# Performance work log

Hardware: AMD Instinct MI355X
Metric: run time of the kernel (lower is better)

The kernel has to match this reference:

```python
import jax, jax.numpy as jnp
import numpy as np

BEAM_WIDTH = 4
BLANK_INDEX = 0
EOS_INDEX = 1


def setup_inputs():
    key = jax.random.key(0)
    k1, k2 = jax.random.split(key)
    T, B, C = 128, 8, 25000
    logits = jax.random.normal(k1, (T, B, C), dtype=jnp.float32)
    seq_len = jnp.full((B,), T, dtype=jnp.int32)
    return {"logits": logits, "seq_len": seq_len}


def _beam_search(logits):
    # logits: [T, B, C]; vectorized form of the per-step beam update:
    #   softmax(beam_score + logits) over C, top-k over (beam, char),
    #   backpointer gather of sequences, per-step re-sort by cumulative log score.
    T, B, C = logits.shape
    W = BEAM_WIDTH
    seqs0 = jnp.full((B, W, T + 1), BLANK_INDEX, dtype=jnp.int32)
    scores0 = jnp.zeros((B, W), dtype=logits.dtype)  # per-step softmax prob score
    logs0 = jnp.zeros((B, W), dtype=logits.dtype)    # accumulated log prob
    active0 = jnp.zeros((B, W), dtype=bool).at[:, 0].set(True)  # start with one beam

    def step(carry, xs):
        scores, logs, seqs, active = carry
        logit_t, t = xs
        # beam score is ADDED to logits before softmax (matches original math)
        expanded = scores[:, :, None] + logit_t[:, None, :]          # [B, W, C]
        probs = jax.nn.softmax(expanded, axis=-1)
        probs = jnp.where(active[:, :, None], probs, -1.0)           # mask inactive beams
        top_p, top_i = jax.lax.top_k(probs.reshape(B, W * C), W)      # [B, W]
        beam_idx = top_i // C                                        # backpointers
        char = (top_i % C).astype(jnp.int32)
        new_logs = jnp.take_along_axis(logs, beam_idx, axis=1) + jnp.log(top_p)
        new_seqs = jnp.take_along_axis(seqs, beam_idx[:, :, None], axis=1)
        # eos is dropped from the sequence in the original; represent as blank
        char_w = jnp.where(char == EOS_INDEX, BLANK_INDEX, char)
        new_seqs = new_seqs.at[:, :, t + 1].set(char_w)
        # per-step re-sort of surviving beams by cumulative log score (desc)
        order = jnp.argsort(-new_logs, axis=1)
        top_p = jnp.take_along_axis(top_p, order, axis=1)
        new_logs = jnp.take_along_axis(new_logs, order, axis=1)
        new_seqs = jnp.take_along_axis(new_seqs, order[:, :, None], axis=1)
        return (top_p, new_logs, new_seqs, jnp.ones_like(active)), None

    (scores, logs, seqs, _), _ = jax.lax.scan(
        step, (scores0, logs0, seqs0, active0), (logits, jnp.arange(T)))
    # final sort by last-step prob score (original sorts by x[0] at the end)
    order = jnp.argsort(-scores, axis=1)
    scores = jnp.take_along_axis(scores, order, axis=1)
    logs = jnp.take_along_axis(logs, order, axis=1)
    seqs = jnp.take_along_axis(seqs, order[:, :, None], axis=1)
    return seqs, scores, logs


def reference(logits, seq_len):
    seqs, scores, logs = _beam_search(logits)
    return seqs, scores, logs
```

## Files before the change

kernel.cpp:

```cpp
#include <hip/hip_runtime.h>
#include <math.h>

#define T_ 128
#define B_ 8
#define C_ 25000
#define W_ 4
#define NROWS (T_ * B_)
#define NT4 (C_ / 4)

__device__ __forceinline__ bool better(float av, int ai, float bv, int bi) {
  return (av > bv) || (av == bv && ai < bi);
}

__global__ __launch_bounds__(512) void rowstats(
    const float* __restrict__ logits,
    float* __restrict__ r_v, int* __restrict__ r_i,
    double* __restrict__ r_p, double* __restrict__ r_lp) {
  const int row = blockIdx.x;
  const float4* __restrict__ x4 =
      reinterpret_cast<const float4*>(logits + (size_t)row * C_);
  const int tid = threadIdx.x;

  float tv[4] = {-INFINITY, -INFINITY, -INFINITY, -INFINITY};
  int ti[4] = {0x7fffffff, 0x7fffffff, 0x7fffffff, 0x7fffffff};
  float s0 = 0.0f, s1 = 0.0f;

  auto ins = [&](float cv, int ci2) {
#pragma unroll
    for (int k = 0; k < 4; ++k) {
      if (better(cv, ci2, tv[k], ti[k])) {
        float t0 = tv[k]; int t1 = ti[k];
        tv[k] = cv; ti[k] = ci2;
        cv = t0; ci2 = t1;
      }
    }
  };

#pragma unroll 4
  for (int i = tid; i < NT4; i += 512) {
    float4 q = x4[i];
    s0 += __expf(q.x) + __expf(q.y);
    s1 += __expf(q.z) + __expf(q.w);
    const int gi = 4 * i;
    if (better(q.x, gi + 0, tv[3], ti[3])) ins(q.x, gi + 0);
    if (better(q.y, gi + 1, tv[3], ti[3])) ins(q.y, gi + 1);
    if (better(q.z, gi + 2, tv[3], ti[3])) ins(q.z, gi + 2);
    if (better(q.w, gi + 3, tv[3], ti[3])) ins(q.w, gi + 3);
  }

  __shared__ float sv[512][4];
  __shared__ int si[512][4];
  __shared__ double ss[512];
#pragma unroll
  for (int k = 0; k < 4; ++k) { sv[tid][k] = tv[k]; si[tid][k] = ti[k]; }
  ss[tid] = (double)s0 + (double)s1;
  __syncthreads();

  for (int off = 256; off > 0; off >>= 1) {
    if (tid < off) {
      ss[tid] += ss[tid + off];
      float a0[4], ov[4]; int a1[4], oi[4];
#pragma unroll
      for (int k = 0; k < 4; ++k) { a0[k] = sv[tid][k]; a1[k] = si[tid][k]; }
      int pa = 0, pb = 0;
#pragma unroll
      for (int k = 0; k < 4; ++k) {
        float bv_ = sv[tid + off][pb]; int bi_ = si[tid + off][pb];
        if (better(a0[pa], a1[pa], bv_, bi_)) { ov[k] = a0[pa]; oi[k] = a1[pa]; ++pa; }
        else { ov[k] = bv_; oi[k] = bi_; ++pb; }
      }
#pragma unroll
      for (int k = 0; k < 4; ++k) { sv[tid][k] = ov[k]; si[tid][k] = oi[k]; }
    }
    __syncthreads();
  }

  if (tid == 0) {
    const int t = row / B_, b = row % B_;
    const int orow = b * T_ + t;
    double den = ss[0];
#pragma unroll
    for (int k = 0; k < 4; ++k) {
      r_v[orow * 4 + k] = sv[0][k];
      r_i[orow * 4 + k] = si[0][k];
      double p = exp((double)sv[0][k]) / den;
      r_p[orow * 4 + k] = p;
      r_lp[orow * 4 + k] = log(p);
    }
  }
}

__global__ __launch_bounds__(64) void beam_sim(
    const float* __restrict__ r_v, const int* __restrict__ r_i,
    const double* __restrict__ r_p, const double* __restrict__ r_lp,
    float* __restrict__ out) {
  const int b = blockIdx.x;
  const int tid = threadIdx.x;

  __shared__ float lv[T_][4];
  __shared__ int lci[T_][4];
  __shared__ double lpk[T_][4];
  __shared__ double lpp[T_][4];
  __shared__ double S[T_];
  __shared__ int Pst[T_][4], Chst[T_][4];
  __shared__ int seq[W_][T_];
  __shared__ double sh_scores[W_], sh_logs[W_];
  __shared__ int sh_ford[W_];

  const size_t base = (size_t)b * T_ * 4;
  for (int e = tid; e < T_ * 4; e += 64) {
    lv[e >> 2][e & 3] = r_v[base + e];
    lci[e >> 2][e & 3] = r_i[base + e];
    lpk[e >> 2][e & 3] = r_lp[base + e];
    lpp[e >> 2][e & 3] = r_p[base + e];
  }
  __syncthreads();

  bool slA = (tid >= 1) &&
      (__float_as_uint(lv[tid][0]) == __float_as_uint(lv[tid][1]));
  bool slB =
      (__float_as_uint(lv[tid + 64][0]) == __float_as_uint(lv[tid + 64][1]));
  const unsigned long long mask0 = __ballot(slA);
  const unsigned long long mask1 = __ballot(slB);

  {
    const int t0 = 2 * tid, t1 = 2 * tid + 1;
    double e0 = (t0 >= 1) ? lpk[t0][0] : 0.0;
    double e1 = lpk[t1][0];
    double pair = e0 + e1;
    double sc = pair;
#pragma unroll
    for (int d = 1; d < 64; d <<= 1) {
      double o = __shfl_up(sc, d, 64);
      if (tid >= d) sc += o;
    }
    double excl = sc - pair;
    S[t0] = excl + e0;
    S[t1] = sc;
  }

  for (int t = tid + 1; t < T_; t += 64) {
    bool slow = (t < 64) ? ((mask0 >> t) & 1ull) : ((mask1 >> (t - 64)) & 1ull);
    if (!slow) {
      int c = lci[t][0];
      seq[0][t] = c; seq[1][t] = c; seq[2][t] = c; seq[3][t] = c;
    }
  }
  __syncthreads();

  if (tid == 0) {
    double logs[4], scor[4] = {0.0, 0.0, 0.0, 0.0};
    for (int j = 0; j < 4; ++j) logs[j] = lpk[0][j];
    int tprev = 0, lastSlow = -1;

    unsigned long long mm = mask0;
    int phase = 0;
    while (true) {
      if (mm == 0) {
        if (phase == 0) { mm = mask1; phase = 1; continue; }
        break;
      }
      int bpos = __builtin_ctzll(mm); mm &= mm - 1;
      int ts = bpos + (phase ? 64 : 0);

      double add = S[ts - 1] - S[tprev];
      for (int j = 0; j < 4; ++j) logs[j] += add;

      float v[4]; int ci[4];
      for (int k = 0; k < 4; ++k) { v[k] = lv[ts][k]; ci[k] = lci[ts][k]; }
      int sw[4], sc_[4], sk[4]; int ns = 0; int k = 0;
      while (ns < 4 && k < 4) {
        int k2 = k;
        while (k2 + 1 < 4 &&
               __float_as_uint(v[k2 + 1]) == __float_as_uint(v[k])) ++k2;
        for (int w = 0; w < 4 && ns < 4; ++w)
          for (int kk = k; kk <= k2 && ns < 4; ++kk) {
            sw[ns] = w; sc_[ns] = ci[kk]; sk[ns] = kk; ++ns;
          }
        k = k2 + 1;
      }
      double nl[4];
      for (int j = 0; j < 4; ++j) nl[j] = logs[sw[j]] + lpk[ts][sk[j]];
      int ord[4] = {0, 1, 2, 3};
      for (int a = 1; a < 4; ++a) {
        int o = ord[a]; int bb = a;
        while (bb > 0 && nl[ord[bb - 1]] < nl[o]) { ord[bb] = ord[bb - 1]; --bb; }
        ord[bb] = o;
      }
      for (int j = 0; j < 4; ++j) {
        Pst[ts][j] = sw[ord[j]];
        Chst[ts][j] = sc_[ord[j]];
      }
      double tl[4];
      for (int j = 0; j < 4; ++j) tl[j] = nl[ord[j]];
      for (int j = 0; j < 4; ++j) logs[j] = tl[j];
      if (ts == T_ - 1)
        for (int j = 0; j < 4; ++j) scor[j] = lpp[ts][sk[ord[j]]];
      tprev = ts;
      lastSlow = ts;
    }
    double add = S[T_ - 1] - S[tprev];
    for (int j = 0; j < 4; ++j) logs[j] += add;
    if (lastSlow != T_ - 1)
      for (int j = 0; j < 4; ++j) scor[j] = lpp[T_ - 1][0];

    float sf[4];
    for (int j = 0; j < 4; ++j) sf[j] = (float)scor[j];
    int ford[4] = {0, 1, 2, 3};
    for (int a = 1; a < 4; ++a) {
      int o = ford[a]; int bb = a;
      while (bb > 0 && sf[ford[bb - 1]] < sf[o]) { ford[bb] = ford[bb - 1]; --bb; }
      ford[bb] = o;
    }
    for (int w = 0; w < 4; ++w) {
      sh_ford[w] = ford[w];
      sh_scores[w] = scor[ford[w]];
      sh_logs[w] = logs[ford[w]];
    }
  }
  __syncthreads();

  if (tid < W_) {
    int j = sh_ford[tid];
    unsigned long long mm = mask1;
    int phase = 1;
    while (true) {
      if (mm == 0) {
        if (phase == 1) { mm = mask0; phase = 0; continue; }
        break;
      }
      int bpos = 63 - __builtin_clzll(mm); mm &= ~(1ull << bpos);
      int ts = bpos + (phase ? 64 : 0);
      seq[tid][ts] = Chst[ts][j];
      j = Pst[ts][j];
    }
    seq[tid][0] = lci[0][j];
  }
  __syncthreads();

  for (int e = tid; e < W_ * (T_ + 1); e += 64) {
    int w = e / (T_ + 1), p = e % (T_ + 1);
    int c = (p == 0) ? 0 : seq[w][p - 1];
    if (c == 1) c = 0;
    out[(size_t)(b * W_ + w) * (T_ + 1) + p] = (float)c;
  }
  if (tid < W_) {
    out[B_ * W_ * (T_ + 1) + b * W_ + tid] = (float)sh_scores[tid];
    out[B_ * W_ * (T_ + 1) + B_ * W_ + b * W_ + tid] = (float)sh_logs[tid];
  }
}

extern "C" void kernel_launch(void* const* d_in, const int* in_sizes, int n_in,
                              void* d_out, int out_size, void* d_ws,
                              size_t ws_size, hipStream_t stream) {
  const float* logits = (const float*)d_in[0];

  char* ws = (char*)d_ws;
  double* r_p = (double*)ws;
  double* r_lp = (double*)(ws + 32768);
  float* r_v = (float*)(ws + 65536);
  int* r_i = (int*)(ws + 81920);
  float* out = (float*)d_out;

  hipLaunchKernelGGL(rowstats, dim3(NROWS), dim3(512), 0, stream,
                     logits, r_v, r_i, r_p, r_lp);
  hipLaunchKernelGGL(beam_sim, dim3(B_), dim3(64), 0, stream,
                     r_v, r_i, r_p, r_lp, out);
}
```

Measured before the change: 46.94 us.

## Compute only top-2 per row, run full top-4 pass only for tied rows

The row-stats kernel now keeps only the max, second max and argmax per thread and reduces them with wave shuffles plus a small cross-wave step, instead of a register top-4 insertion followed by a 9-level shared-memory merge. Only rows whose top two values tie (and the first timestep) re-read the row to build the full top-4. Log-probs are computed as value minus log-denominator. The beam kernel loads compact per-row data and reads top-4 data from global memory only for the slow steps. This cuts the per-element compare/insert work and the shared-memory reduction for most rows, at the cost of a second pass over the data for tied rows.

```diff
diff --git a/kernel.cpp b/kernel.cpp
--- a/kernel.cpp
+++ b/kernel.cpp
@@ -14,51 +14,119 @@
 
 __global__ __launch_bounds__(512) void rowstats(
     const float* __restrict__ logits,
-    float* __restrict__ r_v, int* __restrict__ r_i,
-    double* __restrict__ r_p, double* __restrict__ r_lp) {
+    double* __restrict__ d_lp0, double* __restrict__ d_p0,
+    int* __restrict__ d_ci0, int* __restrict__ d_tied,
+    float* __restrict__ d_t4v, int* __restrict__ d_t4i,
+    double* __restrict__ d_t4lp, double* __restrict__ d_t4p) {
   const int row = blockIdx.x;
   const float4* __restrict__ x4 =
       reinterpret_cast<const float4*>(logits + (size_t)row * C_);
   const int tid = threadIdx.x;
 
-  float tv[4] = {-INFINITY, -INFINITY, -INFINITY, -INFINITY};
-  int ti[4] = {0x7fffffff, 0x7fffffff, 0x7fffffff, 0x7fffffff};
+  float m1 = -INFINITY, m2 = -INFINITY;
+  int idx = 0;
   float s0 = 0.0f, s1 = 0.0f;
-
-  auto ins = [&](float cv, int ci2) {
-#pragma unroll
-    for (int k = 0; k < 4; ++k) {
-      if (better(cv, ci2, tv[k], ti[k])) {
-        float t0 = tv[k]; int t1 = ti[k];
-        tv[k] = cv; ti[k] = ci2;
-        cv = t0; ci2 = t1;
-      }
-    }
-  };
 
 #pragma unroll 4
   for (int i = tid; i < NT4; i += 512) {
     float4 q = x4[i];
+    const int gi = 4 * i;
     s0 += __expf(q.x) + __expf(q.y);
     s1 += __expf(q.z) + __expf(q.w);
+    { bool c = q.x > m1; m2 = fmaxf(m2, fminf(q.x, m1));
+      idx = c ? (gi + 0) : idx; m1 = fmaxf(m1, q.x); }
+    { bool c = q.y > m1; m2 = fmaxf(m2, fminf(q.y, m1));
+      idx = c ? (gi + 1) : idx; m1 = fmaxf(m1, q.y); }
+    { bool c = q.z > m1; m2 = fmaxf(m2, fminf(q.z, m1));
+      idx = c ? (gi + 2) : idx; m1 = fmaxf(m1, q.z); }
+    { bool c = q.w > m1; m2 = fmaxf(m2, fminf(q.w, m1));
+      idx = c ? (gi + 3) : idx; m1 = fmaxf(m1, q.w); }
+  }
+
+  double sumd = (double)s0 + (double)s1;
+#pragma unroll
+  for (int d = 1; d < 64; d <<= 1) {
+    float om1 = __shfl_xor(m1, d, 64);
+    float om2 = __shfl_xor(m2, d, 64);
+    int oidx = __shfl_xor(idx, d, 64);
+    double osum = __shfl_xor(sumd, d, 64);
+    sumd += osum;
+    float nm2 = fmaxf(fminf(m1, om1), fmaxf(m2, om2));
+    bool take = (om1 > m1) || (om1 == m1 && oidx < idx);
+    m1 = take ? om1 : m1;
+    idx = take ? oidx : idx;
+    m2 = nm2;
+  }
+
+  __shared__ float g_m1[8], g_m2[8];
+  __shared__ int g_idx[8];
+  __shared__ double g_sum[8];
+  __shared__ double sh_logden;
+  __shared__ int sh_phase2;
+  if ((tid & 63) == 0) {
+    int w = tid >> 6;
+    g_m1[w] = m1; g_m2[w] = m2; g_idx[w] = idx; g_sum[w] = sumd;
+  }
+  __syncthreads();
+
+  if (tid == 0) {
+    float M1 = g_m1[0], M2 = g_m2[0];
+    int I = g_idx[0];
+    double S = g_sum[0];
+#pragma unroll
+    for (int w = 1; w < 8; ++w) {
+      S += g_sum[w];
+      float b1 = g_m1[w], b2 = g_m2[w];
+      float nm2 = fmaxf(fminf(M1, b1), fmaxf(M2, b2));
+      bool take = (b1 > M1) || (b1 == M1 && g_idx[w] < I);
+      if (take) { M1 = b1; I = g_idx[w]; }
+      M2 = nm2;
+    }
+    const int t = row / B_, b = row % B_;
+    const int orow = b * T_ + t;
+    double logden = log(S);
+    double lp0 = (double)M1 - logden;
+    d_lp0[orow] = lp0;
+    d_p0[orow] = exp(lp0);
+    d_ci0[orow] = I;
+    int tied = (__float_as_uint(M1) == __float_as_uint(M2)) ? 1 : 0;
+    d_tied[orow] = tied;
+    sh_logden = logden;
+    sh_phase2 = tied | (t == 0 ? 1 : 0);
+  }
+  __syncthreads();
+
+  if (!sh_phase2) return;
+
+  float tv[4] = {-INFINITY, -INFINITY, -INFINITY, -INFINITY};
+  int ti4[4] = {0x7fffffff, 0x7fffffff, 0x7fffffff, 0x7fffffff};
+  auto ins = [&](float cv, int ci2) {
+#pragma unroll
+    for (int k = 0; k < 4; ++k) {
+      if (better(cv, ci2, tv[k], ti4[k])) {
+        float t0 = tv[k]; int t1 = ti4[k];
+        tv[k] = cv; ti4[k] = ci2;
+        cv = t0; ci2 = t1;
+      }
+    }
+  };
+  for (int i = tid; i < NT4; i += 512) {
+    float4 q = x4[i];
     const int gi = 4 * i;
-    if (better(q.x, gi + 0, tv[3], ti[3])) ins(q.x, gi + 0);
-    if (better(q.y, gi + 1, tv[3], ti[3])) ins(q.y, gi + 1);
-    if (better(q.z, gi + 2, tv[3], ti[3])) ins(q.z, gi + 2);
-    if (better(q.w, gi + 3, tv[3], ti[3])) ins(q.w, gi + 3);
+    if (better(q.x, gi + 0, tv[3], ti4[3])) ins(q.x, gi + 0);
+    if (better(q.y, gi + 1, tv[3], ti4[3])) ins(q.y, gi + 1);
+    if (better(q.z, gi + 2, tv[3], ti4[3])) ins(q.z, gi + 2);
+    if (better(q.w, gi + 3, tv[3], ti4[3])) ins(q.w, gi + 3);
   }
 
   __shared__ float sv[512][4];
   __shared__ int si[512][4];
-  __shared__ double ss[512];
-#pragma unroll
-  for (int k = 0; k < 4; ++k) { sv[tid][k] = tv[k]; si[tid][k] = ti[k]; }
-  ss[tid] = (double)s0 + (double)s1;
+#pragma unroll
+  for (int k = 0; k < 4; ++k) { sv[tid][k] = tv[k]; si[tid][k] = ti4[k]; }
   __syncthreads();
 
   for (int off = 256; off > 0; off >>= 1) {
     if (tid < off) {
-      ss[tid] += ss[tid + off];
       float a0[4], ov[4]; int a1[4], oi[4];
 #pragma unroll
       for (int k = 0; k < 4; ++k) { a0[k] = sv[tid][k]; a1[k] = si[tid][k]; }
@@ -78,55 +146,53 @@
   if (tid == 0) {
     const int t = row / B_, b = row % B_;
     const int orow = b * T_ + t;
-    double den = ss[0];
+    double logden = sh_logden;
 #pragma unroll
     for (int k = 0; k < 4; ++k) {
-      r_v[orow * 4 + k] = sv[0][k];
-      r_i[orow * 4 + k] = si[0][k];
-      double p = exp((double)sv[0][k]) / den;
-      r_p[orow * 4 + k] = p;
-      r_lp[orow * 4 + k] = log(p);
+      d_t4v[orow * 4 + k] = sv[0][k];
+      d_t4i[orow * 4 + k] = si[0][k];
+      double lp = (double)sv[0][k] - logden;
+      d_t4lp[orow * 4 + k] = lp;
+      d_t4p[orow * 4 + k] = exp(lp);
     }
   }
 }
 
 __global__ __launch_bounds__(64) void beam_sim(
-    const float* __restrict__ r_v, const int* __restrict__ r_i,
-    const double* __restrict__ r_p, const double* __restrict__ r_lp,
+    const double* __restrict__ d_lp0, const double* __restrict__ d_p0,
+    const int* __restrict__ d_ci0, const int* __restrict__ d_tied,
+    const float* __restrict__ d_t4v, const int* __restrict__ d_t4i,
+    const double* __restrict__ d_t4lp, const double* __restrict__ d_t4p,
     float* __restrict__ out) {
   const int b = blockIdx.x;
   const int tid = threadIdx.x;
 
-  __shared__ float lv[T_][4];
-  __shared__ int lci[T_][4];
-  __shared__ double lpk[T_][4];
-  __shared__ double lpp[T_][4];
+  __shared__ double lp0[T_], p0v[T_];
+  __shared__ int ci0[T_], tiedL[T_];
   __shared__ double S[T_];
   __shared__ int Pst[T_][4], Chst[T_][4];
   __shared__ int seq[W_][T_];
   __shared__ double sh_scores[W_], sh_logs[W_];
   __shared__ int sh_ford[W_];
 
-  const size_t base = (size_t)b * T_ * 4;
-  for (int e = tid; e < T_ * 4; e += 64) {
-    lv[e >> 2][e & 3] = r_v[base + e];
-    lci[e >> 2][e & 3] = r_i[base + e];
-    lpk[e >> 2][e & 3] = r_lp[base + e];
-    lpp[e >> 2][e & 3] = r_p[base + e];
-  }
-  __syncthreads();
-
-  bool slA = (tid >= 1) &&
-      (__float_as_uint(lv[tid][0]) == __float_as_uint(lv[tid][1]));
-  bool slB =
-      (__float_as_uint(lv[tid + 64][0]) == __float_as_uint(lv[tid + 64][1]));
+  const int base = b * T_;
+  for (int e = tid; e < T_; e += 64) {
+    lp0[e] = d_lp0[base + e];
+    p0v[e] = d_p0[base + e];
+    ci0[e] = d_ci0[base + e];
+    tiedL[e] = d_tied[base + e];
+  }
+  __syncthreads();
+
+  bool slA = (tid >= 1) && (tiedL[tid] != 0);
+  bool slB = (tiedL[tid + 64] != 0);
   const unsigned long long mask0 = __ballot(slA);
   const unsigned long long mask1 = __ballot(slB);
 
   {
     const int t0 = 2 * tid, t1 = 2 * tid + 1;
-    double e0 = (t0 >= 1) ? lpk[t0][0] : 0.0;
-    double e1 = lpk[t1][0];
+    double e0 = (t0 >= 1) ? lp0[t0] : 0.0;
+    double e1 = lp0[t1];
     double pair = e0 + e1;
     double sc = pair;
 #pragma unroll
@@ -142,7 +208,7 @@
   for (int t = tid + 1; t < T_; t += 64) {
     bool slow = (t < 64) ? ((mask0 >> t) & 1ull) : ((mask1 >> (t - 64)) & 1ull);
     if (!slow) {
-      int c = lci[t][0];
+      int c = ci0[t];
       seq[0][t] = c; seq[1][t] = c; seq[2][t] = c; seq[3][t] = c;
     }
   }
@@ -150,7 +216,8 @@
 
   if (tid == 0) {
     double logs[4], scor[4] = {0.0, 0.0, 0.0, 0.0};
-    for (int j = 0; j < 4; ++j) logs[j] = lpk[0][j];
+    const int base4 = base * 4;
+    for (int j = 0; j < 4; ++j) logs[j] = d_t4lp[base4 + j];
     int tprev = 0, lastSlow = -1;
 
     unsigned long long mm = mask0;
@@ -166,8 +233,14 @@
       double add = S[ts - 1] - S[tprev];
       for (int j = 0; j < 4; ++j) logs[j] += add;
 
-      float v[4]; int ci[4];
-      for (int k = 0; k < 4; ++k) { v[k] = lv[ts][k]; ci[k] = lci[ts][k]; }
+      const int row4 = (base + ts) * 4;
+      float v[4]; int ci[4]; double lpk4[4], pk4[4];
+      for (int k = 0; k < 4; ++k) {
+        v[k] = d_t4v[row4 + k];
+        ci[k] = d_t4i[row4 + k];
+        lpk4[k] = d_t4lp[row4 + k];
+        pk4[k] = d_t4p[row4 + k];
+      }
       int sw[4], sc_[4], sk[4]; int ns = 0; int k = 0;
       while (ns < 4 && k < 4) {
         int k2 = k;
@@ -180,7 +253,7 @@
         k = k2 + 1;
       }
       double nl[4];
-      for (int j = 0; j < 4; ++j) nl[j] = logs[sw[j]] + lpk[ts][sk[j]];
+      for (int j = 0; j < 4; ++j) nl[j] = logs[sw[j]] + lpk4[sk[j]];
       int ord[4] = {0, 1, 2, 3};
       for (int a = 1; a < 4; ++a) {
         int o = ord[a]; int bb = a;
@@ -195,14 +268,14 @@
       for (int j = 0; j < 4; ++j) tl[j] = nl[ord[j]];
       for (int j = 0; j < 4; ++j) logs[j] = tl[j];
       if (ts == T_ - 1)
-        for (int j = 0; j < 4; ++j) scor[j] = lpp[ts][sk[ord[j]]];
+        for (int j = 0; j < 4; ++j) scor[j] = pk4[sk[ord[j]]];
       tprev = ts;
       lastSlow = ts;
     }
     double add = S[T_ - 1] - S[tprev];
     for (int j = 0; j < 4; ++j) logs[j] += add;
     if (lastSlow != T_ - 1)
-      for (int j = 0; j < 4; ++j) scor[j] = lpp[T_ - 1][0];
+      for (int j = 0; j < 4; ++j) scor[j] = p0v[T_ - 1];
 
     float sf[4];
     for (int j = 0; j < 4; ++j) sf[j] = (float)scor[j];
@@ -234,7 +307,7 @@
       seq[tid][ts] = Chst[ts][j];
       j = Pst[ts][j];
     }
-    seq[tid][0] = lci[0][j];
+    seq[tid][0] = d_t4i[base * 4 + j];
   }
   __syncthreads();
 
@@ -256,14 +329,20 @@
   const float* logits = (const float*)d_in[0];
 
   char* ws = (char*)d_ws;
-  double* r_p = (double*)ws;
-  double* r_lp = (double*)(ws + 32768);
-  float* r_v = (float*)(ws + 65536);
-  int* r_i = (int*)(ws + 81920);
+  double* d_lp0 = (double*)(ws + 0);
+  double* d_p0 = (double*)(ws + 8192);
+  double* d_t4lp = (double*)(ws + 16384);
+  double* d_t4p = (double*)(ws + 49152);
+  int* d_ci0 = (int*)(ws + 81920);
+  int* d_tied = (int*)(ws + 86016);
+  float* d_t4v = (float*)(ws + 90112);
+  int* d_t4i = (int*)(ws + 106496);
   float* out = (float*)d_out;
 
   hipLaunchKernelGGL(rowstats, dim3(NROWS), dim3(512), 0, stream,
-                     logits, r_v, r_i, r_p, r_lp);
+                     logits, d_lp0, d_p0, d_ci0, d_tied,
+                     d_t4v, d_t4i, d_t4lp, d_t4p);
   hipLaunchKernelGGL(beam_sim, dim3(B_), dim3(64), 0, stream,
-                     r_v, r_i, r_p, r_lp, out);
+                     d_lp0, d_p0, d_ci0, d_tied,
+                     d_t4v, d_t4i, d_t4lp, d_t4p, out);
 }
```

Result: faster. 41.72 us (-11.1%).
